# Kernel optimization log

Hardware: AMD Instinct MI355X
Metric: run time of the kernel (lower is better)

## Reference

```python
import jax, jax.numpy as jnp
import numpy as np

N_VOX = 500_000
C = 128
HID = 4 * C
RES = 128  # voxel grid resolution
K_OFFS = 27


def _build_sparse_coords_and_neighbors(seed=0):
    rng = np.random.default_rng(seed)
    lin = rng.choice(RES ** 3, size=N_VOX, replace=False)
    z = lin // (RES * RES)
    y = (lin // RES) % RES
    x = lin % RES
    # padded grid (RES+2)^3 so boundary lookups are in-bounds
    P = RES + 2
    grid = -np.ones(P * P * P, dtype=np.int64)
    z1, y1, x1 = z + 1, y + 1, x + 1
    grid[z1 * P * P + y1 * P + x1] = np.arange(N_VOX)
    offs = np.array([[dz, dy, dx] for dz in (-1, 0, 1) for dy in (-1, 0, 1) for dx in (-1, 0, 1)], dtype=np.int64)  # [27,3]
    nz = z1[:, None] + offs[None, :, 0]
    ny = y1[:, None] + offs[None, :, 1]
    nx = x1[:, None] + offs[None, :, 2]
    nbr = grid[nz * P * P + ny * P + nx]  # [N,27], -1 if neighbor voxel inactive
    return nbr.astype(np.int32)


def setup_inputs() -> dict:
    key = jax.random.key(0)
    ks = jax.random.split(key, 8)
    nbr = _build_sparse_coords_and_neighbors()
    scale = 0.02
    return {
        "feats": jax.random.normal(ks[0], (N_VOX, C), jnp.float32),
        "neighbor_idx": jnp.asarray(nbr),
        "conv_w": jax.random.normal(ks[1], (K_OFFS, C, C), jnp.float32) * scale,
        "conv_b": jax.random.normal(ks[2], (C,), jnp.float32) * scale,
        "ln_g": jnp.ones((C,), jnp.float32),
        "ln_b": jnp.zeros((C,), jnp.float32),
        "w1": jax.random.normal(ks[3], (C, HID), jnp.float32) * scale,
        "b1": jax.random.normal(ks[4], (HID,), jnp.float32) * scale,
        "w2": jax.random.normal(ks[5], (HID, C), jnp.float32) * scale,
        "b2": jax.random.normal(ks[6], (C,), jnp.float32) * scale,
    }


def _forward(feats, neighbor_idx, conv_w, conv_b, ln_g, ln_b, w1, b1, w2, b2):
    n, c = feats.shape
    # submanifold sparse conv3d: pad a zero row for missing (-1) neighbors
    f_pad = jnp.concatenate([feats, jnp.zeros((1, c), feats.dtype)], axis=0)
    idx = jnp.where(neighbor_idx < 0, n, neighbor_idx)  # [N,27]
    h = jnp.broadcast_to(conv_b, (n, c))
    for k in range(K_OFFS):  # fixed small kernel-offset loop; per-offset gather + GEMM
        h = h + f_pad[idx[:, k]] @ conv_w[k]
    # LayerNorm32 (fp32 math), eps=1e-6, affine
    h32 = h.astype(jnp.float32)
    mu = h32.mean(-1, keepdims=True)
    var = h32.var(-1, keepdims=True)
    hn = ((h32 - mu) * jax.lax.rsqrt(var + 1e-6) * ln_g + ln_b).astype(feats.dtype)
    # MLP: Linear -> SiLU -> Linear
    m = jax.nn.silu(hn @ w1 + b1) @ w2 + b2
    # residual h + x on sparse feats
    return m + feats


def reference(feats, neighbor_idx, conv_w, conv_b, ln_g, ln_b, w1, b1, w2, b2):
    return _forward(feats, neighbor_idx, conv_w, conv_b, ln_g, ln_b, w1, b1, w2, b2)
```

## Files before the change

### kernel.cpp

```cpp
#include <hip/hip_runtime.h>
#include <stdint.h>

#define NVOX 500000
#define NPAD 500224
#define ZERO_OFF (NVOX * 128)

typedef float  f32x4  __attribute__((ext_vector_type(4)));
typedef short  short8 __attribute__((ext_vector_type(8)));

__device__ __forceinline__ short f2bf(float x){
  unsigned u = __float_as_uint(x);
  unsigned r = (u + 0x7fffu + ((u >> 16) & 1u)) >> 16;
  return (short)r;
}

__device__ __forceinline__ int cvt_pk_bf16(float lo, float hi){
  int r;
  asm("v_cvt_pk_bf16_f32 %0, %1, %2" : "=v"(r) : "v"(lo), "v"(hi));
  return r;
}

__device__ __forceinline__ void gload_lds16(const void* g, void* l){
  __builtin_amdgcn_global_load_lds(
      (const __attribute__((address_space(1))) unsigned int*)(uintptr_t)g,
      (__attribute__((address_space(3))) unsigned int*)(unsigned int)(uintptr_t)l,
      16, 0, 0);
}

__global__ void cast_feats_kernel(const float* __restrict__ f, short* __restrict__ t){
  long i = ((long)blockIdx.x * 256 + threadIdx.x) * 8;
  float4 a = *(const float4*)(f + i);
  float4 b = *(const float4*)(f + i + 4);
  short8 o = { f2bf(a.x), f2bf(a.y), f2bf(a.z), f2bf(a.w),
               f2bf(b.x), f2bf(b.y), f2bf(b.z), f2bf(b.w) };
  *(short8*)(t + i) = o;
}

__global__ void prep_nbr_kernel(const int* __restrict__ nbr, int* __restrict__ nbrT){
  __shared__ int lds_n[6912];
  const int tid = threadIdx.x;
  const long base = (long)blockIdx.x * 6912;
  #pragma unroll
  for (int i = 0; i < 27; i++){
    long g = base + i*256 + tid;
    lds_n[i*256 + tid] = (g < (long)NVOX*27) ? nbr[g] : -1;
  }
  __syncthreads();
  const int row = blockIdx.x * 256 + tid;
  #pragma unroll
  for (int k = 0; k < 27; k++){
    int id = lds_n[tid*27 + k];
    nbrT[(size_t)k*NPAD + row] = (id < 0 ? NVOX : id) * 128;
  }
}

__global__ void prep_weights_kernel(const float* __restrict__ cw, const float* __restrict__ w1,
                                    const float* __restrict__ w2,
                                    short* __restrict__ cw_sw, short* __restrict__ w1_sw,
                                    short* __restrict__ w2_sw){
  int t = blockIdx.x * 256 + threadIdx.x;
  if (t < 55296){
    int k = t >> 11, rem = t & 2047;
    int nf = rem >> 8, ks = (rem >> 6) & 3, l = rem & 63;
    int g = l >> 4, c = l & 15;
    short8 o;
    #pragma unroll
    for (int j = 0; j < 8; j++){
      int kk = ks*32 + g*8 + j;
      o[j] = f2bf(cw[(k*128 + kk)*128 + nf*16 + c]);
    }
    size_t dst = (size_t)(k*2 + (ks >> 1))*8192 + (size_t)(nf*2 + (ks & 1))*512 + (size_t)l*8;
    *(short8*)(cw_sw + dst) = o;
  } else if (t < 63488){
    int u = t - 55296;
    int nf = u >> 8, ks = (u >> 6) & 3, l = u & 63;
    int g = l >> 4, c = l & 15;
    short8 o;
    #pragma unroll
    for (int j = 0; j < 8; j++){
      int kk = ks*32 + g*8 + j;
      o[j] = f2bf(w1[kk*512 + nf*16 + c]);
    }
    *(short8*)(w1_sw + (size_t)u*8) = o;
  } else {
    int u = t - 63488;
    int c32 = u >> 9, nf = (u >> 6) & 7, l = u & 63;
    int g = l >> 4, c = l & 15;
    short8 o;
    #pragma unroll
    for (int j = 0; j < 8; j++){
      int k = c32*32 + g*8 + j;
      o[j] = f2bf(w2[k*128 + nf*16 + c]);
    }
    *(short8*)(w2_sw + (size_t)u*8) = o;
  }
}

__global__ __launch_bounds__(256, 4)
void conv_ln_v4_kernel(const short* __restrict__ table, const int* __restrict__ nbrT,
                       const short* __restrict__ cw_sw,
                       const float* __restrict__ conv_b, const float* __restrict__ ln_g,
                       const float* __restrict__ ln_b, short* __restrict__ hn16){
  __shared__ __align__(16) short lds_b[2][8192];
  const int tid = threadIdx.x;
  const int lane = tid & 63, wv = tid >> 6;
  const int l15 = lane & 15, lg = lane >> 4;
  const int rowbase = blockIdx.x * 128 + wv * 32;
  const int rowi = rowbase + l15;

  f32x4 acc[2][8];
  #pragma unroll
  for (int m = 0; m < 2; m++)
    #pragma unroll
    for (int n = 0; n < 8; n++)
      acc[m][n] = f32x4{0.f, 0.f, 0.f, 0.f};

  int idx_c[2], idx_n[2];
  #pragma unroll
  for (int m = 0; m < 2; m++) idx_c[m] = __builtin_nontemporal_load(&nbrT[rowi + m*16]);
  #pragma unroll
  for (int m = 0; m < 2; m++) idx_n[m] = __builtin_nontemporal_load(&nbrT[NPAD + rowi + m*16]);

  {
    const char* src = (const char*)cw_sw;
    char* dst = (char*)&lds_b[0][0];
    #pragma unroll
    for (int i = 0; i < 4; i++){ int off = i*4096 + tid*16; gload_lds16(src+off, dst+off); }
  }

  for (int k = 0; k < 27; k++){
    __syncthreads();
    {
      const char* src = (const char*)cw_sw + (size_t)(k*2 + 1)*16384;
      char* dst = (char*)&lds_b[1][0];
      #pragma unroll
      for (int i = 0; i < 4; i++){ int off = i*4096 + tid*16; gload_lds16(src+off, dst+off); }
    }
    {
      short8 af0[2], af1[2];
      #pragma unroll
      for (int m = 0; m < 2; m++)
        af0[m] = *(const short8*)(table + (size_t)(unsigned)idx_c[m] + lg*8);
      #pragma unroll
      for (int m = 0; m < 2; m++)
        af1[m] = *(const short8*)(table + (size_t)(unsigned)idx_c[m] + 32 + lg*8);
      const short* b0 = &lds_b[0][0];
      #pragma unroll
      for (int n = 0; n < 8; n++){
        short8 b = *(const short8*)(b0 + ((n*2 + 0)*64 + lane)*8);
        #pragma unroll
        for (int m = 0; m < 2; m++)
          acc[m][n] = __builtin_amdgcn_mfma_f32_16x16x32_bf16(af0[m], b, acc[m][n], 0, 0, 0);
      }
      #pragma unroll
      for (int n = 0; n < 8; n++){
        short8 b = *(const short8*)(b0 + ((n*2 + 1)*64 + lane)*8);
        #pragma unroll
        for (int m = 0; m < 2; m++)
          acc[m][n] = __builtin_amdgcn_mfma_f32_16x16x32_bf16(af1[m], b, acc[m][n], 0, 0, 0);
      }
    }
    __syncthreads();
    if (k + 1 < 27){
      const char* src = (const char*)cw_sw + (size_t)(k+1)*32768;
      char* dst = (char*)&lds_b[0][0];
      #pragma unroll
      for (int i = 0; i < 4; i++){ int off = i*4096 + tid*16; gload_lds16(src+off, dst+off); }
    }
    int idx_n2[2];
    #pragma unroll
    for (int m = 0; m < 2; m++)
      idx_n2[m] = (k + 2 < 27) ? __builtin_nontemporal_load(&nbrT[(size_t)(k+2)*NPAD + rowi + m*16])
                               : ZERO_OFF;
    {
      short8 af2[2], af3[2];
      #pragma unroll
      for (int m = 0; m < 2; m++)
        af2[m] = *(const short8*)(table + (size_t)(unsigned)idx_c[m] + 64 + lg*8);
      #pragma unroll
      for (int m = 0; m < 2; m++)
        af3[m] = *(const short8*)(table + (size_t)(unsigned)idx_c[m] + 96 + lg*8);
      const short* b1 = &lds_b[1][0];
      #pragma unroll
      for (int n = 0; n < 8; n++){
        short8 b = *(const short8*)(b1 + ((n*2 + 0)*64 + lane)*8);
        #pragma unroll
        for (int m = 0; m < 2; m++)
          acc[m][n] = __builtin_amdgcn_mfma_f32_16x16x32_bf16(af2[m], b, acc[m][n], 0, 0, 0);
      }
      #pragma unroll
      for (int n = 0; n < 8; n++){
        short8 b = *(const short8*)(b1 + ((n*2 + 1)*64 + lane)*8);
        #pragma unroll
        for (int m = 0; m < 2; m++)
          acc[m][n] = __builtin_amdgcn_mfma_f32_16x16x32_bf16(af3[m], b, acc[m][n], 0, 0, 0);
      }
    }
    #pragma unroll
    for (int m = 0; m < 2; m++){ idx_c[m] = idx_n[m]; idx_n[m] = idx_n2[m]; }
  }

  float cb[8], g8[8], be[8];
  #pragma unroll
  for (int n = 0; n < 8; n++){
    cb[n] = conv_b[n*16 + l15];
    g8[n] = ln_g[n*16 + l15];
    be[n] = ln_b[n*16 + l15];
  }
  #pragma unroll
  for (int m = 0; m < 2; m++){
    #pragma unroll
    for (int r = 0; r < 4; r++){
      float s = 0.f, s2 = 0.f;
      #pragma unroll
      for (int n = 0; n < 8; n++){
        float h = acc[m][n][r] + cb[n];
        acc[m][n][r] = h;
        s += h; s2 += h*h;
      }
      #pragma unroll
      for (int msk = 1; msk < 16; msk <<= 1){
        s  += __shfl_xor(s,  msk);
        s2 += __shfl_xor(s2, msk);
      }
      float mu  = s  * 0.0078125f;
      float var = s2 * 0.0078125f - mu*mu;
      float rs  = rsqrtf(var + 1e-6f);
      int row = rowbase + m*16 + lg*4 + r;
      if (row < NVOX){
        #pragma unroll
        for (int n = 0; n < 8; n++){
          float hv = (acc[m][n][r] - mu) * rs * g8[n] + be[n];
          __builtin_nontemporal_store(f2bf(hv), &hn16[(size_t)row*128 + n*16 + l15]);
        }
      }
    }
  }
}

template<bool TBL>
__global__ __launch_bounds__(256, 2)
void conv_ln_kernel(const short* __restrict__ table, const float* __restrict__ feats,
                    const int* __restrict__ nbr, const short* __restrict__ cw_sw,
                    const float* __restrict__ conv_b, const float* __restrict__ ln_g,
                    const float* __restrict__ ln_b, short* __restrict__ hn16){
  __shared__ __align__(16) short lds_b[2][16384];
  const int tid = threadIdx.x;
  const int lane = tid & 63, wv = tid >> 6;
  const int l15 = lane & 15, lg = lane >> 4;
  const int rowbase = blockIdx.x * 256 + wv * 64;

  f32x4 acc[4][8];
  #pragma unroll
  for (int m = 0; m < 4; m++)
    #pragma unroll
    for (int n = 0; n < 8; n++)
      acc[m][n] = f32x4{0.f, 0.f, 0.f, 0.f};

  {
    const char* src = (const char*)cw_sw;
    char* dst = (char*)&lds_b[0][0];
    #pragma unroll
    for (int i = 0; i < 8; i++){ int off = i*4096 + tid*16; gload_lds16(src+off, dst+off); }
  }

  for (int k = 0; k < 27; k++){
    const int buf = k & 1;
    __syncthreads();
    if (k + 1 < 27){
      const char* src = (const char*)cw_sw + (size_t)(k+1)*32768;
      char* dst = (char*)&lds_b[buf ^ 1][0];
      #pragma unroll
      for (int i = 0; i < 8; i++){ int off = i*4096 + tid*16; gload_lds16(src+off, dst+off); }
    }
    int idxr[4];
    #pragma unroll
    for (int m = 0; m < 4; m++){
      int row = rowbase + m*16 + l15;
      row = row < NVOX ? row : NVOX - 1;
      int id = nbr[row*27 + k];
      idxr[m] = TBL ? (id < 0 ? NVOX : id) : id;
    }
    const short* bbase = &lds_b[buf][0];
    #pragma unroll
    for (int ks = 0; ks < 4; ks++){
      short8 af[4];
      #pragma unroll
      for (int m = 0; m < 4; m++){
        if constexpr (TBL){
          af[m] = *(const short8*)(table + (size_t)idxr[m]*128 + ks*32 + lg*8);
        } else {
          if (idxr[m] < 0){
            af[m] = short8{0,0,0,0,0,0,0,0};
          } else {
            const float* p = feats + (size_t)idxr[m]*128 + ks*32 + lg*8;
            float4 x = *(const float4*)p;
            float4 y = *(const float4*)(p + 4);
            af[m] = short8{ f2bf(x.x), f2bf(x.y), f2bf(x.z), f2bf(x.w),
                            f2bf(y.x), f2bf(y.y), f2bf(y.z), f2bf(y.w) };
          }
        }
      }
      #pragma unroll
      for (int n = 0; n < 8; n++){
        short8 b = *(const short8*)(bbase + (ks >> 1)*8192 + (((n*2 + (ks & 1))*64) + lane)*8);
        #pragma unroll
        for (int m = 0; m < 4; m++)
          acc[m][n] = __builtin_amdgcn_mfma_f32_16x16x32_bf16(af[m], b, acc[m][n], 0, 0, 0);
      }
    }
  }

  float cb[8], g8[8], be[8];
  #pragma unroll
  for (int n = 0; n < 8; n++){
    cb[n] = conv_b[n*16 + l15];
    g8[n] = ln_g[n*16 + l15];
    be[n] = ln_b[n*16 + l15];
  }
  #pragma unroll
  for (int m = 0; m < 4; m++){
    #pragma unroll
    for (int r = 0; r < 4; r++){
      float s = 0.f, s2 = 0.f;
      #pragma unroll
      for (int n = 0; n < 8; n++){
        float h = acc[m][n][r] + cb[n];
        acc[m][n][r] = h;
        s += h; s2 += h*h;
      }
      #pragma unroll
      for (int msk = 1; msk < 16; msk <<= 1){
        s  += __shfl_xor(s,  msk);
        s2 += __shfl_xor(s2, msk);
      }
      float mu  = s  * 0.0078125f;
      float var = s2 * 0.0078125f - mu*mu;
      float rs  = rsqrtf(var + 1e-6f);
      int row = rowbase + m*16 + lg*4 + r;
      if (row < NVOX){
        #pragma unroll
        for (int n = 0; n < 8; n++){
          float hv = (acc[m][n][r] - mu) * rs * g8[n] + be[n];
          hn16[(size_t)row*128 + n*16 + l15] = f2bf(hv);
        }
      }
    }
  }
}

__global__ __launch_bounds__(256, 3)
void mlp_kernel(const short* __restrict__ hn16, const float* __restrict__ feats,
                const short* __restrict__ w1_sw, const short* __restrict__ w2_sw,
                const float* __restrict__ b1, const float* __restrict__ b2,
                float* __restrict__ out){
  __shared__ __align__(16) short lds_w[2][8192];
  const int tid = threadIdx.x;
  const int lane = tid & 63, wv = tid >> 6;
  const int l15 = lane & 15, lg = lane >> 4;
  const int rowbase = blockIdx.x * 128 + wv * 32;
  const int sl0 = l15 + 32*(lg & 1);
  const int sl1 = sl0 + 16;
  const bool hiHalf = (lg >> 1) != 0;

  f32x4 acc2[2][8];
  #pragma unroll
  for (int m = 0; m < 2; m++)
    #pragma unroll
    for (int n = 0; n < 8; n++)
      acc2[m][n] = f32x4{0.f, 0.f, 0.f, 0.f};

  int rowg[2];
  #pragma unroll
  for (int m = 0; m < 2; m++){
    int row = rowbase + m*16 + l15;
    rowg[m] = row < NVOX ? row : NVOX - 1;
  }

  short8 a1[4][2];
  #pragma unroll
  for (int ks = 0; ks < 4; ks++)
    #pragma unroll
    for (int m = 0; m < 2; m++)
      a1[ks][m] = *(const short8*)(hn16 + (size_t)rowg[m]*128 + ks*32 + lg*8);

  {
    const char* s1 = (const char*)w1_sw;
    const char* s2 = (const char*)w2_sw;
    char* dst = (char*)&lds_w[0][0];
    #pragma unroll
    for (int i = 0; i < 2; i++){ int off = i*4096 + tid*16; gload_lds16(s1+off, dst+off); }
    #pragma unroll
    for (int i = 0; i < 2; i++){ int off = i*4096 + tid*16; gload_lds16(s2+off, dst+8192+off); }
  }

  for (int ch = 0; ch < 16; ch++){
    const int buf = ch & 1;
    __syncthreads();
    if (ch + 1 < 16){
      const char* s1 = (const char*)w1_sw + (size_t)(ch+1)*8192;
      const char* s2 = (const char*)w2_sw + (size_t)(ch+1)*8192;
      char* dst = (char*)&lds_w[buf ^ 1][0];
      #pragma unroll
      for (int i = 0; i < 2; i++){ int off = i*4096 + tid*16; gload_lds16(s1+off, dst+off); }
      #pragma unroll
      for (int i = 0; i < 2; i++){ int off = i*4096 + tid*16; gload_lds16(s2+off, dst+8192+off); }
    }
    const short* w1c = &lds_w[buf][0];
    const short* w2c = &lds_w[buf][4096];

    float4 b1v0 = *(const float4*)(b1 + ch*32 +  0 + lg*4);
    float4 b1v1 = *(const float4*)(b1 + ch*32 + 16 + lg*4);

    f32x4 p00 = f32x4{0.f,0.f,0.f,0.f}, p01 = f32x4{0.f,0.f,0.f,0.f};
    f32x4 p10 = f32x4{0.f,0.f,0.f,0.f}, p11 = f32x4{0.f,0.f,0.f,0.f};
    #pragma unroll
    for (int ks = 0; ks < 4; ks++){
      short8 wA0 = *(const short8*)(w1c + ((0*4 + ks)*64 + lane)*8);
      short8 wA1 = *(const short8*)(w1c + ((1*4 + ks)*64 + lane)*8);
      p00 = __builtin_amdgcn_mfma_f32_16x16x32_bf16(wA0, a1[ks][0], p00, 0, 0, 0);
      p01 = __builtin_amdgcn_mfma_f32_16x16x32_bf16(wA0, a1[ks][1], p01, 0, 0, 0);
      p10 = __builtin_amdgcn_mfma_f32_16x16x32_bf16(wA1, a1[ks][0], p10, 0, 0, 0);
      p11 = __builtin_amdgcn_mfma_f32_16x16x32_bf16(wA1, a1[ks][1], p11, 0, 0, 0);
    }

    int pk00[2], pk01[2], pk10[2], pk11[2];
    {
      float s0, s1v, s2v, s3;
      #define SILU4(P, BV, PK)                                            \
        s0 = (P)[0] + (BV).x; s0 = s0 / (1.f + __expf(-s0));              \
        s1v = (P)[1] + (BV).y; s1v = s1v / (1.f + __expf(-s1v));          \
        s2v = (P)[2] + (BV).z; s2v = s2v / (1.f + __expf(-s2v));          \
        s3 = (P)[3] + (BV).w; s3 = s3 / (1.f + __expf(-s3));              \
        (PK)[0] = cvt_pk_bf16(s0, s1v); (PK)[1] = cvt_pk_bf16(s2v, s3);
      SILU4(p00, b1v0, pk00)
      SILU4(p01, b1v0, pk01)
      SILU4(p10, b1v1, pk10)
      SILU4(p11, b1v1, pk11)
      #undef SILU4
    }

    union { int i[4]; short8 s; } a2u0, a2u1;
    #pragma unroll
    for (int w = 0; w < 4; w++){
      int src = (w < 2) ? sl0 : sl1;
      int t0 = __shfl(pk00[w & 1], src);
      int t1 = __shfl(pk10[w & 1], src);
      a2u0.i[w] = hiHalf ? t1 : t0;
      int u0 = __shfl(pk01[w & 1], src);
      int u1 = __shfl(pk11[w & 1], src);
      a2u1.i[w] = hiHalf ? u1 : u0;
    }

    #pragma unroll
    for (int n = 0; n < 8; n++){
      short8 b = *(const short8*)(w2c + (n*64 + lane)*8);
      acc2[0][n] = __builtin_amdgcn_mfma_f32_16x16x32_bf16(a2u0.s, b, acc2[0][n], 0, 0, 0);
      acc2[1][n] = __builtin_amdgcn_mfma_f32_16x16x32_bf16(a2u1.s, b, acc2[1][n], 0, 0, 0);
    }
  }

  float bb2[8];
  #pragma unroll
  for (int n = 0; n < 8; n++) bb2[n] = b2[n*16 + l15];
  #pragma unroll
  for (int m = 0; m < 2; m++)
    #pragma unroll
    for (int n = 0; n < 8; n++)
      #pragma unroll
      for (int r = 0; r < 4; r++){
        int row = rowbase + m*16 + lg*4 + r;
        if (row < NVOX){
          size_t ci = (size_t)row*128 + n*16 + l15;
          out[ci] = acc2[m][n][r] + bb2[n] + feats[ci];
        }
      }
}

extern "C" void kernel_launch(void* const* d_in, const int* in_sizes, int n_in,
                              void* d_out, int out_size, void* d_ws, size_t ws_size,
                              hipStream_t stream){
  const float* feats = (const float*)d_in[0];
  const int*   nbr   = (const int*)  d_in[1];
  const float* cw    = (const float*)d_in[2];
  const float* cb    = (const float*)d_in[3];
  const float* lng   = (const float*)d_in[4];
  const float* lnb   = (const float*)d_in[5];
  const float* w1    = (const float*)d_in[6];
  const float* b1    = (const float*)d_in[7];
  const float* w2    = (const float*)d_in[8];
  const float* b2    = (const float*)d_in[9];
  float* out = (float*)d_out;

  char* ws = (char*)d_ws;
  const size_t TABLE_B = (size_t)(NVOX + 1) * 256;
  const size_t HN_B    = (size_t)NVOX * 256;
  const size_t CW_B    = 55296u * 16u;
  const size_t W1_B    = 8192u * 16u;
  const size_t W2_B    = 8192u * 16u;
  const size_t NBRT_B  = (size_t)27 * NPAD * 4;
  const size_t need_full = TABLE_B + HN_B + CW_B + W1_B + W2_B;
  const size_t need_pf   = need_full + NBRT_B;

  if (ws_size >= need_pf){
    short* table = (short*)ws;
    short* hn16  = (short*)(ws + TABLE_B);
    short* cw_sw = (short*)(ws + TABLE_B + HN_B);
    short* w1_sw = (short*)(ws + TABLE_B + HN_B + CW_B);
    short* w2_sw = (short*)(ws + TABLE_B + HN_B + CW_B + W1_B);
    int*   nbrT  = (int*)  (ws + need_full);

    cast_feats_kernel<<<31250, 256, 0, stream>>>(feats, table);
    hipMemsetAsync((void*)(table + (size_t)NVOX * 128), 0, 256, stream);
    prep_nbr_kernel<<<1954, 256, 0, stream>>>(nbr, nbrT);
    prep_weights_kernel<<<280, 256, 0, stream>>>(cw, w1, w2, cw_sw, w1_sw, w2_sw);
    conv_ln_v4_kernel<<<3907, 256, 0, stream>>>(table, nbrT, cw_sw, cb, lng, lnb, hn16);
    mlp_kernel<<<3907, 256, 0, stream>>>(hn16, feats, w1_sw, w2_sw, b1, b2, out);
  } else if (ws_size >= need_full){
    short* table = (short*)ws;
    short* hn16  = (short*)(ws + TABLE_B);
    short* cw_sw = (short*)(ws + TABLE_B + HN_B);
    short* w1_sw = (short*)(ws + TABLE_B + HN_B + CW_B);
    short* w2_sw = (short*)(ws + TABLE_B + HN_B + CW_B + W1_B);

    cast_feats_kernel<<<31250, 256, 0, stream>>>(feats, table);
    hipMemsetAsync((void*)(table + (size_t)NVOX * 128), 0, 256, stream);
    prep_weights_kernel<<<280, 256, 0, stream>>>(cw, w1, w2, cw_sw, w1_sw, w2_sw);
    conv_ln_kernel<true><<<1954, 256, 0, stream>>>(table, feats, nbr, cw_sw, cb, lng, lnb, hn16);
    mlp_kernel<<<3907, 256, 0, stream>>>(hn16, feats, w1_sw, w2_sw, b1, b2, out);
  } else {
    short* hn16  = (short*)ws;
    short* cw_sw = (short*)(ws + HN_B);
    short* w1_sw = (short*)(ws + HN_B + CW_B);
    short* w2_sw = (short*)(ws + HN_B + CW_B + W1_B);

    prep_weights_kernel<<<280, 256, 0, stream>>>(cw, w1, w2, cw_sw, w1_sw, w2_sw);
    conv_ln_kernel<false><<<1954, 256, 0, stream>>>(nullptr, feats, nbr, cw_sw, cb, lng, lnb, hn16);
    mlp_kernel<<<3907, 256, 0, stream>>>(hn16, feats, w1_sw, w2_sw, b1, b2, out);
  }
}
```

Before: 855.0 us.

## Fuse conv+LayerNorm with MLP in one kernel, keeping normalized tile in LDS

Measured after the change: 892.5 us. 4.4% more time.

```diff
diff --git a/kernel.cpp b/kernel.cpp
--- a/kernel.cpp
+++ b/kernel.cpp
@@ -96,12 +96,15 @@
   }
 }
 
-__global__ __launch_bounds__(256, 4)
-void conv_ln_v4_kernel(const short* __restrict__ table, const int* __restrict__ nbrT,
-                       const short* __restrict__ cw_sw,
-                       const float* __restrict__ conv_b, const float* __restrict__ ln_g,
-                       const float* __restrict__ ln_b, short* __restrict__ hn16){
-  __shared__ __align__(16) short lds_b[2][8192];
+__global__ __launch_bounds__(256, 3)
+void fused_kernel(const short* __restrict__ table, const int* __restrict__ nbrT,
+                  const short* __restrict__ cw_sw,
+                  const float* __restrict__ conv_b, const float* __restrict__ ln_g,
+                  const float* __restrict__ ln_b,
+                  const short* __restrict__ w1_sw, const short* __restrict__ w2_sw,
+                  const float* __restrict__ b1, const float* __restrict__ b2,
+                  const float* __restrict__ feats, float* __restrict__ out){
+  __shared__ __align__(16) short lds[16384];
   const int tid = threadIdx.x;
   const int lane = tid & 63, wv = tid >> 6;
   const int l15 = lane & 15, lg = lane >> 4;
@@ -123,7 +126,7 @@
 
   {
     const char* src = (const char*)cw_sw;
-    char* dst = (char*)&lds_b[0][0];
+    char* dst = (char*)&lds[0];
     #pragma unroll
     for (int i = 0; i < 4; i++){ int off = i*4096 + tid*16; gload_lds16(src+off, dst+off); }
   }
@@ -132,7 +135,7 @@
     __syncthreads();
     {
       const char* src = (const char*)cw_sw + (size_t)(k*2 + 1)*16384;
-      char* dst = (char*)&lds_b[1][0];
+      char* dst = (char*)&lds[8192];
       #pragma unroll
       for (int i = 0; i < 4; i++){ int off = i*4096 + tid*16; gload_lds16(src+off, dst+off); }
     }
@@ -144,7 +147,7 @@
       #pragma unroll
       for (int m = 0; m < 2; m++)
         af1[m] = *(const short8*)(table + (size_t)(unsigned)idx_c[m] + 32 + lg*8);
-      const short* b0 = &lds_b[0][0];
+      const short* b0 = &lds[0];
       #pragma unroll
       for (int n = 0; n < 8; n++){
         short8 b = *(const short8*)(b0 + ((n*2 + 0)*64 + lane)*8);
@@ -163,7 +166,7 @@
     __syncthreads();
     if (k + 1 < 27){
       const char* src = (const char*)cw_sw + (size_t)(k+1)*32768;
-      char* dst = (char*)&lds_b[0][0];
+      char* dst = (char*)&lds[0];
       #pragma unroll
       for (int i = 0; i < 4; i++){ int off = i*4096 + tid*16; gload_lds16(src+off, dst+off); }
     }
@@ -180,17 +183,17 @@
       #pragma unroll
       for (int m = 0; m < 2; m++)
         af3[m] = *(const short8*)(table + (size_t)(unsigned)idx_c[m] + 96 + lg*8);
-      const short* b1 = &lds_b[1][0];
+      const short* b1p = &lds[8192];
       #pragma unroll
       for (int n = 0; n < 8; n++){
-        short8 b = *(const short8*)(b1 + ((n*2 + 0)*64 + lane)*8);
+        short8 b = *(const short8*)(b1p + ((n*2 + 0)*64 + lane)*8);
         #pragma unroll
         for (int m = 0; m < 2; m++)
           acc[m][n] = __builtin_amdgcn_mfma_f32_16x16x32_bf16(af2[m], b, acc[m][n], 0, 0, 0);
       }
       #pragma unroll
       for (int n = 0; n < 8; n++){
-        short8 b = *(const short8*)(b1 + ((n*2 + 1)*64 + lane)*8);
+        short8 b = *(const short8*)(b1p + ((n*2 + 1)*64 + lane)*8);
         #pragma unroll
         for (int m = 0; m < 2; m++)
           acc[m][n] = __builtin_amdgcn_mfma_f32_16x16x32_bf16(af3[m], b, acc[m][n], 0, 0, 0);
@@ -200,42 +203,156 @@
     for (int m = 0; m < 2; m++){ idx_c[m] = idx_n[m]; idx_n[m] = idx_n2[m]; }
   }
 
-  float cb[8], g8[8], be[8];
-  #pragma unroll
-  for (int n = 0; n < 8; n++){
-    cb[n] = conv_b[n*16 + l15];
-    g8[n] = ln_g[n*16 + l15];
-    be[n] = ln_b[n*16 + l15];
-  }
-  #pragma unroll
-  for (int m = 0; m < 2; m++){
-    #pragma unroll
-    for (int r = 0; r < 4; r++){
-      float s = 0.f, s2 = 0.f;
-      #pragma unroll
-      for (int n = 0; n < 8; n++){
-        float h = acc[m][n][r] + cb[n];
-        acc[m][n][r] = h;
-        s += h; s2 += h*h;
-      }
-      #pragma unroll
-      for (int msk = 1; msk < 16; msk <<= 1){
-        s  += __shfl_xor(s,  msk);
-        s2 += __shfl_xor(s2, msk);
-      }
-      float mu  = s  * 0.0078125f;
-      float var = s2 * 0.0078125f - mu*mu;
-      float rs  = rsqrtf(var + 1e-6f);
-      int row = rowbase + m*16 + lg*4 + r;
-      if (row < NVOX){
+  __syncthreads();
+  short* hnw = &lds[wv * 4096];
+  {
+    float cb[8], g8[8], be[8];
+    #pragma unroll
+    for (int n = 0; n < 8; n++){
+      cb[n] = conv_b[n*16 + l15];
+      g8[n] = ln_g[n*16 + l15];
+      be[n] = ln_b[n*16 + l15];
+    }
+    #pragma unroll
+    for (int m = 0; m < 2; m++){
+      #pragma unroll
+      for (int r = 0; r < 4; r++){
+        float s = 0.f, s2 = 0.f;
+        #pragma unroll
+        for (int n = 0; n < 8; n++){
+          float h = acc[m][n][r] + cb[n];
+          acc[m][n][r] = h;
+          s += h; s2 += h*h;
+        }
+        #pragma unroll
+        for (int msk = 1; msk < 16; msk <<= 1){
+          s  += __shfl_xor(s,  msk);
+          s2 += __shfl_xor(s2, msk);
+        }
+        float mu  = s  * 0.0078125f;
+        float var = s2 * 0.0078125f - mu*mu;
+        float rs  = rsqrtf(var + 1e-6f);
+        int rowloc = m*16 + lg*4 + r;
         #pragma unroll
         for (int n = 0; n < 8; n++){
           float hv = (acc[m][n][r] - mu) * rs * g8[n] + be[n];
-          __builtin_nontemporal_store(f2bf(hv), &hn16[(size_t)row*128 + n*16 + l15]);
+          hnw[(rowloc*128 + n*16 + l15) ^ ((rowloc & 7) << 3)] = f2bf(hv);
         }
       }
     }
   }
+
+  short8 a1[4][2];
+  #pragma unroll
+  for (int ks = 0; ks < 4; ks++)
+    #pragma unroll
+    for (int m = 0; m < 2; m++){
+      int rowloc = m*16 + l15;
+      a1[ks][m] = *(const short8*)(hnw + ((rowloc*128 + ks*32 + lg*8) ^ ((rowloc & 7) << 3)));
+    }
+  __syncthreads();
+
+  #pragma unroll
+  for (int m = 0; m < 2; m++)
+    #pragma unroll
+    for (int n = 0; n < 8; n++)
+      acc[m][n] = f32x4{0.f, 0.f, 0.f, 0.f};
+
+  const int sl0 = l15 + 32*(lg & 1);
+  const int sl1 = sl0 + 16;
+  const bool hiHalf = (lg >> 1) != 0;
+
+  {
+    const char* s1 = (const char*)w1_sw;
+    const char* s2 = (const char*)w2_sw;
+    char* dst = (char*)&lds[0];
+    #pragma unroll
+    for (int i = 0; i < 2; i++){ int off = i*4096 + tid*16; gload_lds16(s1+off, dst+off); }
+    #pragma unroll
+    for (int i = 0; i < 2; i++){ int off = i*4096 + tid*16; gload_lds16(s2+off, dst+8192+off); }
+  }
+
+  for (int ch = 0; ch < 16; ch++){
+    const int buf = ch & 1;
+    __syncthreads();
+    if (ch + 1 < 16){
+      const char* s1 = (const char*)w1_sw + (size_t)(ch+1)*8192;
+      const char* s2 = (const char*)w2_sw + (size_t)(ch+1)*8192;
+      char* dst = (char*)&lds[(buf ^ 1) * 8192];
+      #pragma unroll
+      for (int i = 0; i < 2; i++){ int off = i*4096 + tid*16; gload_lds16(s1+off, dst+off); }
+      #pragma unroll
+      for (int i = 0; i < 2; i++){ int off = i*4096 + tid*16; gload_lds16(s2+off, dst+8192+off); }
+    }
+    const short* w1c = &lds[buf * 8192];
+    const short* w2c = w1c + 4096;
+
+    float4 b1v0 = *(const float4*)(b1 + ch*32 +  0 + lg*4);
+    float4 b1v1 = *(const float4*)(b1 + ch*32 + 16 + lg*4);
+
+    f32x4 p00 = f32x4{0.f,0.f,0.f,0.f}, p01 = f32x4{0.f,0.f,0.f,0.f};
+    f32x4 p10 = f32x4{0.f,0.f,0.f,0.f}, p11 = f32x4{0.f,0.f,0.f,0.f};
+    #pragma unroll
+    for (int ks = 0; ks < 4; ks++){
+      short8 wA0 = *(const short8*)(w1c + ((0*4 + ks)*64 + lane)*8);
+      short8 wA1 = *(const short8*)(w1c + ((1*4 + ks)*64 + lane)*8);
+      p00 = __builtin_amdgcn_mfma_f32_16x16x32_bf16(wA0, a1[ks][0], p00, 0, 0, 0);
+      p01 = __builtin_amdgcn_mfma_f32_16x16x32_bf16(wA0, a1[ks][1], p01, 0, 0, 0);
+      p10 = __builtin_amdgcn_mfma_f32_16x16x32_bf16(wA1, a1[ks][0], p10, 0, 0, 0);
+      p11 = __builtin_amdgcn_mfma_f32_16x16x32_bf16(wA1, a1[ks][1], p11, 0, 0, 0);
+    }
+
+    int pk00[2], pk01[2], pk10[2], pk11[2];
+    {
+      float s0, s1v, s2v, s3;
+      #define SILU4(P, BV, PK)                                            \
+        s0 = (P)[0] + (BV).x; s0 = s0 / (1.f + __expf(-s0));              \
+        s1v = (P)[1] + (BV).y; s1v = s1v / (1.f + __expf(-s1v));          \
+        s2v = (P)[2] + (BV).z; s2v = s2v / (1.f + __expf(-s2v));          \
+        s3 = (P)[3] + (BV).w; s3 = s3 / (1.f + __expf(-s3));              \
+        (PK)[0] = cvt_pk_bf16(s0, s1v); (PK)[1] = cvt_pk_bf16(s2v, s3);
+      SILU4(p00, b1v0, pk00)
+      SILU4(p01, b1v0, pk01)
+      SILU4(p10, b1v1, pk10)
+      SILU4(p11, b1v1, pk11)
+      #undef SILU4
+    }
+
+    union { int i[4]; short8 s; } a2u0, a2u1;
+    #pragma unroll
+    for (int w = 0; w < 4; w++){
+      int src = (w < 2) ? sl0 : sl1;
+      int t0 = __shfl(pk00[w & 1], src);
+      int t1 = __shfl(pk10[w & 1], src);
+      a2u0.i[w] = hiHalf ? t1 : t0;
+      int u0 = __shfl(pk01[w & 1], src);
+      int u1 = __shfl(pk11[w & 1], src);
+      a2u1.i[w] = hiHalf ? u1 : u0;
+    }
+
+    #pragma unroll
+    for (int n = 0; n < 8; n++){
+      short8 b = *(const short8*)(w2c + (n*64 + lane)*8);
+      acc[0][n] = __builtin_amdgcn_mfma_f32_16x16x32_bf16(a2u0.s, b, acc[0][n], 0, 0, 0);
+      acc[1][n] = __builtin_amdgcn_mfma_f32_16x16x32_bf16(a2u1.s, b, acc[1][n], 0, 0, 0);
+    }
+  }
+
+  float bb2[8];
+  #pragma unroll
+  for (int n = 0; n < 8; n++) bb2[n] = b2[n*16 + l15];
+  #pragma unroll
+  for (int m = 0; m < 2; m++)
+    #pragma unroll
+    for (int n = 0; n < 8; n++)
+      #pragma unroll
+      for (int r = 0; r < 4; r++){
+        int row = rowbase + m*16 + lg*4 + r;
+        if (row < NVOX){
+          size_t ci = (size_t)row*128 + n*16 + l15;
+          out[ci] = acc[m][n][r] + bb2[n] + feats[ci];
+        }
+      }
 }
 
 template<bool TBL>
@@ -499,23 +616,22 @@
   const size_t W1_B    = 8192u * 16u;
   const size_t W2_B    = 8192u * 16u;
   const size_t NBRT_B  = (size_t)27 * NPAD * 4;
-  const size_t need_full = TABLE_B + HN_B + CW_B + W1_B + W2_B;
-  const size_t need_pf   = need_full + NBRT_B;
-
-  if (ws_size >= need_pf){
+  const size_t need_fused = TABLE_B + CW_B + W1_B + W2_B + NBRT_B;
+  const size_t need_full  = TABLE_B + HN_B + CW_B + W1_B + W2_B;
+
+  if (ws_size >= need_fused){
     short* table = (short*)ws;
-    short* hn16  = (short*)(ws + TABLE_B);
-    short* cw_sw = (short*)(ws + TABLE_B + HN_B);
-    short* w1_sw = (short*)(ws + TABLE_B + HN_B + CW_B);
-    short* w2_sw = (short*)(ws + TABLE_B + HN_B + CW_B + W1_B);
-    int*   nbrT  = (int*)  (ws + need_full);
+    short* cw_sw = (short*)(ws + TABLE_B);
+    short* w1_sw = (short*)(ws + TABLE_B + CW_B);
+    short* w2_sw = (short*)(ws + TABLE_B + CW_B + W1_B);
+    int*   nbrT  = (int*)  (ws + TABLE_B + CW_B + W1_B + W2_B);
 
     cast_feats_kernel<<<31250, 256, 0, stream>>>(feats, table);
     hipMemsetAsync((void*)(table + (size_t)NVOX * 128), 0, 256, stream);
     prep_nbr_kernel<<<1954, 256, 0, stream>>>(nbr, nbrT);
     prep_weights_kernel<<<280, 256, 0, stream>>>(cw, w1, w2, cw_sw, w1_sw, w2_sw);
-    conv_ln_v4_kernel<<<3907, 256, 0, stream>>>(table, nbrT, cw_sw, cb, lng, lnb, hn16);
-    mlp_kernel<<<3907, 256, 0, stream>>>(hn16, feats, w1_sw, w2_sw, b1, b2, out);
+    fused_kernel<<<3907, 256, 0, stream>>>(table, nbrT, cw_sw, cb, lng, lnb,
+                                           w1_sw, w2_sw, b1, b2, feats, out);
   } else if (ws_size >= need_full){
     short* table = (short*)ws;
     short* hn16  = (short*)(ws + TABLE_B);
```
